# Kernel optimization log

Measured on AMD Instinct MI355X. Metric: run time of the kernel, lower is better.

## Reference

```python
import jax, jax.numpy as jnp
import numpy as np

HEADS = 8
DIM_HEADS = 64
M_DIM = 512
X_DIM = 512
MEM_NUM = 512
N = 16384
PERCENT = 0.25
LAY_NUMBER = 2       # outer refinement iterations
CROSS_LAYERS = 2     # layers inside M_cross_layers
EPS = 1e-5


def setup_inputs() -> dict:
    key = jax.random.key(0)
    ks = jax.random.split(key, 8)
    data = jax.random.normal(ks[0], (N, X_DIM), dtype=jnp.float32)
    Memory = jax.random.normal(ks[1], (MEM_NUM, M_DIM), dtype=jnp.float32)
    # to_kv: Linear(X_dim, 2*kv_dim, bias=False); kv_dim = heads*dim_heads
    Wkv = jax.random.normal(ks[2], (X_DIM, 2 * HEADS * DIM_HEADS), dtype=jnp.float32) * 0.02
    # per cross layer: to_q (no bias) and mutl_heads (with bias)
    Wq = jax.random.normal(ks[3], (CROSS_LAYERS, M_DIM, HEADS * DIM_HEADS), dtype=jnp.float32) * 0.02
    Wm = jax.random.normal(ks[4], (CROSS_LAYERS, HEADS * DIM_HEADS, M_DIM), dtype=jnp.float32) * 0.02
    bm = jnp.zeros((CROSS_LAYERS, M_DIM), dtype=jnp.float32)
    return {"data": data, "Memory": Memory, "Wkv": Wkv, "Wq": Wq, "Wm": Wm, "bm": bm, "istest": 0}


def _layer_norm(x):
    # F.layer_norm over last dim, no affine params
    mu = jnp.mean(x, axis=-1, keepdims=True)
    var = jnp.var(x, axis=-1, keepdims=True)
    return (x - mu) * jax.lax.rsqrt(var + EPS)


def _cross_layer(M, X, Wkv, Wq_l, Wm_l, bm_l):
    # cross_att + residual + layernorm (SublayerConnection); FFN is dead code in source
    q = (M @ Wq_l).reshape(MEM_NUM, HEADS, DIM_HEADS).transpose(1, 0, 2)      # [h, m, dh]
    kv = X @ Wkv                                                              # [n, 2*h*dh]
    k, v = jnp.split(kv, 2, axis=-1)
    k = k.reshape(-1, HEADS, DIM_HEADS).transpose(1, 0, 2)                    # [h, n, dh]
    v = v.reshape(-1, HEADS, DIM_HEADS).transpose(1, 0, 2)
    sim = jnp.einsum('hid,hjd->hij', q, k) * (DIM_HEADS ** -0.5)              # [h, m, n]
    att = jax.nn.softmax(sim, axis=-1)
    o = jnp.einsum('hij,hjd->hid', att, v)                                    # [h, m, dh]
    o = o.transpose(1, 0, 2).reshape(MEM_NUM, HEADS * DIM_HEADS)
    out = o @ Wm_l + bm_l                                                     # [m, M_dim]
    return _layer_norm(out + M)


def _cross_layers(M, X, Wkv, Wq, Wm, bm):
    for l in range(CROSS_LAYERS):
        M = _cross_layer(M, X, Wkv, Wq[l], Wm[l], bm[l])
    return M


def _calucate_sim(data, M):
    # per-sample landmark similarity: max scaled dot product against memory rows
    logits = (data @ M.T) * (DIM_HEADS ** -0.5)   # [N, mem]
    return jnp.max(logits, axis=-1)               # [N]


def _calucate_emb(data, M):
    logits = (data @ M.T) * (DIM_HEADS ** -0.5)   # [N, mem]
    logp = jax.nn.log_softmax(logits, axis=-1)
    p = jnp.exp(logp)
    out_ebs = p @ M                               # soft memory readout [N, M_dim]
    result_loss = -jnp.mean(jnp.max(logp, axis=-1))
    lse = jax.scipy.special.logsumexp(logits, axis=-1)
    zloss = jnp.mean(lse ** 2)                    # router-style z-loss
    return out_ebs, result_loss, zloss


def _select(data, sim_M, k):
    _, top_idx = jax.lax.top_k(sim_M, k)
    X = jnp.zeros_like(data)
    return X.at[top_idx].set(data[top_idx])


def reference(data, Memory, Wkv, Wq, Wm, bm, istest):
    M = Memory
    sim_M = _calucate_sim(data, M)
    percent_count = int(data.shape[0] * PERCENT)
    if not istest:
        X = _select(data, sim_M, percent_count)
        for _ in range(LAY_NUMBER):
            M = _cross_layers(M, X, Wkv, Wq, Wm, bm)
            sim_M = _calucate_sim(data, M)
            X = _select(data, sim_M, percent_count)
    out_ebs, result_loss, zloss = _calucate_emb(data, M)
    return (sim_M, out_ebs, result_loss, zloss)
```

## Files before the change

### kernel.cpp

```cpp
#include <hip/hip_runtime.h>
#include <cstdint>

#define N_DATA 16384
#define DIM 512
#define MEM 512
#define KSEL 4096
#define NH 8
#define DH 64
#define KVDIM 1024
#define SCALE 0.125f
#define ZCNT 12288.0f
#define LN_EPS 1e-5f
#define NSPLIT 4

typedef unsigned short u16;
using short8 = __attribute__((ext_vector_type(8))) short;
using f32x4  = __attribute__((ext_vector_type(4))) float;

__device__ __forceinline__ unsigned fenc(float x) {
    unsigned u = __float_as_uint(x);
    return (u & 0x80000000u) ? ~u : (u | 0x80000000u);
}
__device__ __forceinline__ u16 f2bf(float x) {
    unsigned u = __float_as_uint(x);
    u += 0x7fffu + ((u >> 16) & 1u);
    return (u16)(u >> 16);
}
__device__ __forceinline__ float bf2f(u16 h) { return __uint_as_float(((unsigned)h) << 16); }

__device__ __forceinline__ float waveSum(float v) {
#pragma unroll
    for (int o = 32; o > 0; o >>= 1) v += __shfl_down(v, o, 64);
    return v;
}
__device__ float blockSum(float v) {
    __shared__ float sh[4];
    __syncthreads();
    v = waveSum(v);
    if ((threadIdx.x & 63) == 0) sh[threadIdx.x >> 6] = v;
    __syncthreads();
    if (threadIdx.x == 0) { float s = sh[0]; for (int i = 1; i < 4; ++i) s += sh[i]; sh[0] = s; }
    __syncthreads();
    return sh[0];
}

template<int ROWS, int NW, bool GATHER>
__device__ __forceinline__ void stage_tile(const u16* __restrict__ src, int ld, int k0,
                                           int row0, const int* __restrict__ gidx,
                                           u16* lds, int wave)
{
    constexpr int NI = ROWS / 16;
    const int lane = threadIdx.x & 63;
#pragma unroll
    for (int i = wave; i < NI; i += NW) {
        const int ch = i * 64 + lane;
        const int r = ch >> 2, cc = ch & 3;
        int rg = row0 + r;
        if (GATHER) rg = gidx[rg];
        const u16* g = src + (long)rg * ld + k0 + cc * 8;
        u16* l = lds + i * 512;
        __builtin_amdgcn_global_load_lds((const __attribute__((address_space(1))) void*)g,
                                         (__attribute__((address_space(3))) void*)l,
                                         16, 0, 0);
    }
}

template<int WM, int WN, bool GATHER, int EPI, bool BIAS>
__global__ __launch_bounds__(WM * WN * 64)
void mfma_gemm(const u16* __restrict__ A, const u16* __restrict__ B,
               const float* __restrict__ bias, const int* __restrict__ gidx,
               void* __restrict__ Cv, unsigned* __restrict__ simenc,
               u16* __restrict__ vTo,
               int K, int lda, int ldb, int ldc,
               long zsA, long zsB, long zsC, int zdiv, long zsplitC, float alpha)
{
    constexpr int BM = WM * 64, BN = WN * 64, NW = WM * WN;
    __shared__ __align__(16) u16 As[BM * 32];
    __shared__ __align__(16) u16 Bs[BN * 32];

    const int t = threadIdx.x;
    const int wave = t >> 6, lane = t & 63;
    const int wr = wave / WN, wc = wave % WN;
    const int l15 = lane & 15, l4 = lane >> 4;
    const int bm0 = blockIdx.x * BM, bn0 = blockIdx.y * BN;
    const int zs = (int)blockIdx.z % zdiv;
    const int zh = (int)blockIdx.z / zdiv;
    A += (long)zh * zsA;
    B += (long)zh * zsB;

    f32x4 acc[4][4];
#pragma unroll
    for (int i = 0; i < 4; ++i)
#pragma unroll
        for (int j = 0; j < 4; ++j)
#pragma unroll
            for (int r = 0; r < 4; ++r) acc[i][j][r] = 0.f;

    const int Kd = K / zdiv;
    const int kbeg = zs * Kd;
    for (int k0 = kbeg; k0 < kbeg + Kd; k0 += 32) {
        stage_tile<BM, NW, GATHER>(A, lda, k0, bm0, gidx, As, wave);
        stage_tile<BN, NW, false>(B, ldb, k0, bn0, nullptr, Bs, wave);
        __syncthreads();
        short8 a[4], b[4];
#pragma unroll
        for (int fm = 0; fm < 4; ++fm)
            a[fm] = *(const short8*)(As + (wr * 64 + fm * 16 + l15) * 32 + l4 * 8);
#pragma unroll
        for (int fn = 0; fn < 4; ++fn)
            b[fn] = *(const short8*)(Bs + (wc * 64 + fn * 16 + l15) * 32 + l4 * 8);
#pragma unroll
        for (int fm = 0; fm < 4; ++fm)
#pragma unroll
            for (int fn = 0; fn < 4; ++fn)
                acc[fm][fn] = __builtin_amdgcn_mfma_f32_16x16x32_bf16(a[fm], b[fn], acc[fm][fn], 0, 0, 0);
        __syncthreads();
    }

    if (EPI == 2) {
#pragma unroll
        for (int fm = 0; fm < 4; ++fm)
#pragma unroll
            for (int r = 0; r < 4; ++r) {
                float mx = acc[fm][0][r];
#pragma unroll
                for (int fn = 1; fn < 4; ++fn) mx = fmaxf(mx, acc[fm][fn][r]);
#pragma unroll
                for (int o = 8; o >= 1; o >>= 1) mx = fmaxf(mx, __shfl_xor(mx, o, 64));
                if (l15 == 0) {
                    const int row = bm0 + wr * 64 + fm * 16 + l4 * 4 + r;
                    atomicMax(simenc + row, fenc(alpha * mx));
                }
            }
    } else if (EPI == 0) {
        float* C = (float*)Cv + (long)zh * zsC + (long)zs * zsplitC;
#pragma unroll
        for (int fm = 0; fm < 4; ++fm)
#pragma unroll
            for (int fn = 0; fn < 4; ++fn)
#pragma unroll
                for (int r = 0; r < 4; ++r) {
                    const int row = bm0 + wr * 64 + fm * 16 + l4 * 4 + r;
                    const int col = bn0 + wc * 64 + fn * 16 + l15;
                    float v = alpha * acc[fm][fn][r];
                    if (BIAS) v += bias[col];
                    C[(long)row * ldc + col] = v;
                }
    } else if (EPI == 1) {
        u16* C = (u16*)Cv + (long)zh * zsC + (long)zs * zsplitC;
#pragma unroll
        for (int fm = 0; fm < 4; ++fm)
#pragma unroll
            for (int fn = 0; fn < 4; ++fn)
#pragma unroll
                for (int r = 0; r < 4; ++r) {
                    const int row = bm0 + wr * 64 + fm * 16 + l4 * 4 + r;
                    const int col = bn0 + wc * 64 + fn * 16 + l15;
                    float v = alpha * acc[fm][fn][r];
                    if (BIAS) v += bias[col];
                    C[(long)row * ldc + col] = f2bf(v);
                }
    } else {
        if (bn0 < 512) {
            u16* C = (u16*)Cv;
#pragma unroll
            for (int fm = 0; fm < 4; ++fm)
#pragma unroll
                for (int fn = 0; fn < 4; ++fn)
#pragma unroll
                    for (int r = 0; r < 4; ++r) {
                        const int row = bm0 + wr * 64 + fm * 16 + l4 * 4 + r;
                        const int col = bn0 + wc * 64 + fn * 16 + l15;
                        C[(long)row * ldc + col] = f2bf(alpha * acc[fm][fn][r]);
                    }
        } else {
#pragma unroll
            for (int fm = 0; fm < 4; ++fm)
#pragma unroll
                for (int fn = 0; fn < 4; ++fn) {
                    const int d = bn0 + wc * 64 + fn * 16 + l15 - 512;
                    const int row0 = bm0 + wr * 64 + fm * 16 + l4 * 4;
                    ushort4 pw;
                    pw.x = f2bf(alpha * acc[fm][fn][0]);
                    pw.y = f2bf(alpha * acc[fm][fn][1]);
                    pw.z = f2bf(alpha * acc[fm][fn][2]);
                    pw.w = f2bf(alpha * acc[fm][fn][3]);
                    *(ushort4*)(vTo + (long)d * 4096 + row0) = pw;
                }
        }
    }
}

__global__ __launch_bounds__(512)
void mfma_gemm_sm(const u16* __restrict__ A, const u16* __restrict__ B,
                  u16* __restrict__ Obf, float* __restrict__ simf,
                  float* __restrict__ lse, float* __restrict__ mlp, float alpha)
{
    __shared__ __align__(16) u16 As[64 * 32];
    __shared__ __align__(16) u16 Bs[512 * 32];
    const int t = threadIdx.x, wave = t >> 6, lane = t & 63;
    const int wc = wave;
    const int l15 = lane & 15, l4 = lane >> 4;
    const int bm0 = blockIdx.x * 64;

    f32x4 acc[4][4];
#pragma unroll
    for (int i = 0; i < 4; ++i)
#pragma unroll
        for (int j = 0; j < 4; ++j)
#pragma unroll
            for (int r = 0; r < 4; ++r) acc[i][j][r] = 0.f;

    for (int k0 = 0; k0 < 512; k0 += 32) {
        stage_tile<64, 8, false>(A, 512, k0, bm0, nullptr, As, wave);
        stage_tile<512, 8, false>(B, 512, k0, 0, nullptr, Bs, wave);
        __syncthreads();
        short8 a[4], b[4];
#pragma unroll
        for (int fm = 0; fm < 4; ++fm)
            a[fm] = *(const short8*)(As + (fm * 16 + l15) * 32 + l4 * 8);
#pragma unroll
        for (int fn = 0; fn < 4; ++fn)
            b[fn] = *(const short8*)(Bs + (wc * 64 + fn * 16 + l15) * 32 + l4 * 8);
#pragma unroll
        for (int fm = 0; fm < 4; ++fm)
#pragma unroll
            for (int fn = 0; fn < 4; ++fn)
                acc[fm][fn] = __builtin_amdgcn_mfma_f32_16x16x32_bf16(a[fm], b[fn], acc[fm][fn], 0, 0, 0);
        __syncthreads();
    }

    float* red  = (float*)As;
    float* rowv = (float*)Bs;

#pragma unroll
    for (int fm = 0; fm < 4; ++fm)
#pragma unroll
        for (int r = 0; r < 4; ++r) {
            float mx = alpha * acc[fm][0][r];
#pragma unroll
            for (int fn = 1; fn < 4; ++fn) mx = fmaxf(mx, alpha * acc[fm][fn][r]);
#pragma unroll
            for (int o = 1; o <= 8; o <<= 1) mx = fmaxf(mx, __shfl_xor(mx, o, 64));
            if (l15 == 0) red[(fm * 16 + l4 * 4 + r) * 8 + wc] = mx;
        }
    __syncthreads();
    if (t < 64) {
        float mx = red[t * 8];
#pragma unroll
        for (int j = 1; j < 8; ++j) mx = fmaxf(mx, red[t * 8 + j]);
        rowv[t] = mx;
    }
    __syncthreads();
#pragma unroll
    for (int fm = 0; fm < 4; ++fm)
#pragma unroll
        for (int r = 0; r < 4; ++r) {
            const int rl = fm * 16 + l4 * 4 + r;
            const float m = rowv[rl];
            float s = 0.f;
#pragma unroll
            for (int fn = 0; fn < 4; ++fn) s += __expf(alpha * acc[fm][fn][r] - m);
#pragma unroll
            for (int o = 1; o <= 8; o <<= 1) s += __shfl_xor(s, o, 64);
            if (l15 == 0) red[rl * 8 + wc] = s;
        }
    __syncthreads();
    if (t < 64) {
        float s = 0.f;
#pragma unroll
        for (int j = 0; j < 8; ++j) s += red[t * 8 + j];
        const float m = rowv[t];
        const float l = m + __logf(s);
        const int gr = bm0 + t;
        simf[gr] = m; lse[gr] = l; mlp[gr] = m - l;
        rowv[64 + t] = l;
    }
    __syncthreads();
#pragma unroll
    for (int fm = 0; fm < 4; ++fm)
#pragma unroll
        for (int r = 0; r < 4; ++r) {
            const int rl = fm * 16 + l4 * 4 + r;
            const float l = rowv[64 + rl];
#pragma unroll
            for (int fn = 0; fn < 4; ++fn) {
                const int col = wc * 64 + fn * 16 + l15;
                Obf[(long)(bm0 + rl) * 512 + col] = f2bf(__expf(alpha * acc[fm][fn][r] - l));
            }
        }
}

__global__ __launch_bounds__(512)
void wmln(const u16* __restrict__ A, const u16* __restrict__ BT,
          const float* __restrict__ bias, const float* __restrict__ Min,
          float* __restrict__ Mout, u16* __restrict__ Mbf)
{
    __shared__ __align__(16) u16 As[16 * 32];
    __shared__ __align__(16) u16 Bs[512 * 32];
    __shared__ float red[16][8], red2[16][8], rowv[32];
    const int t = threadIdx.x, wave = t >> 6, lane = t & 63;
    const int wc = wave;
    const int l15 = lane & 15, l4 = lane >> 4;
    const int bm0 = blockIdx.x * 16;

    f32x4 acc[4];
#pragma unroll
    for (int fn = 0; fn < 4; ++fn)
#pragma unroll
        for (int r = 0; r < 4; ++r) acc[fn][r] = 0.f;

    for (int k0 = 0; k0 < 512; k0 += 32) {
        stage_tile<16, 8, false>(A, 512, k0, bm0, nullptr, As, wave);
        stage_tile<512, 8, false>(BT, 512, k0, 0, nullptr, Bs, wave);
        __syncthreads();
        const short8 a = *(const short8*)(As + l15 * 32 + l4 * 8);
#pragma unroll
        for (int fn = 0; fn < 4; ++fn) {
            const short8 b = *(const short8*)(Bs + (wc * 64 + fn * 16 + l15) * 32 + l4 * 8);
            acc[fn] = __builtin_amdgcn_mfma_f32_16x16x32_bf16(a, b, acc[fn], 0, 0, 0);
        }
        __syncthreads();
    }

    float v[4][4];
#pragma unroll
    for (int fn = 0; fn < 4; ++fn) {
        const int col = wc * 64 + fn * 16 + l15;
        const float bi = bias[col];
#pragma unroll
        for (int r = 0; r < 4; ++r) {
            const int row = bm0 + l4 * 4 + r;
            v[fn][r] = acc[fn][r] + bi + Min[(long)row * 512 + col];
        }
    }
#pragma unroll
    for (int r = 0; r < 4; ++r) {
        float s = 0.f, s2 = 0.f;
#pragma unroll
        for (int fn = 0; fn < 4; ++fn) { const float x = v[fn][r]; s += x; s2 += x * x; }
#pragma unroll
        for (int o = 1; o <= 8; o <<= 1) { s += __shfl_xor(s, o, 64); s2 += __shfl_xor(s2, o, 64); }
        if (l15 == 0) { red[l4 * 4 + r][wc] = s; red2[l4 * 4 + r][wc] = s2; }
    }
    __syncthreads();
    if (t < 16) {
        float s = 0.f, s2 = 0.f;
#pragma unroll
        for (int j = 0; j < 8; ++j) { s += red[t][j]; s2 += red2[t][j]; }
        const float mu = s * (1.f / 512.f);
        const float var = s2 * (1.f / 512.f) - mu * mu;
        rowv[t] = mu;
        rowv[16 + t] = rsqrtf(var + LN_EPS);
    }
    __syncthreads();
#pragma unroll
    for (int fn = 0; fn < 4; ++fn) {
        const int col = wc * 64 + fn * 16 + l15;
#pragma unroll
        for (int r = 0; r < 4; ++r) {
            const int rl = l4 * 4 + r;
            const float y = (v[fn][r] - rowv[rl]) * rowv[16 + rl];
            Mout[(long)(bm0 + rl) * 512 + col] = y;
            Mbf [(long)(bm0 + rl) * 512 + col] = f2bf(y);
        }
    }
}

__global__ __launch_bounds__(256)
void flash_att(const u16* __restrict__ Mbf, const u16* __restrict__ WqT,
               const u16* __restrict__ KV, const u16* __restrict__ VT,
               float* __restrict__ oPart, float* __restrict__ mPart,
               float* __restrict__ lPart)
{
    __shared__ __align__(16) u16 Qs[64 * 64];
    __shared__ __align__(16) u16 Ks[2][64 * 64];
    __shared__ __align__(16) u16 Vs[2][64 * 64];
    __shared__ __align__(16) u16 Ps[4][16 * 72];

    const int qt = blockIdx.x, h = blockIdx.y, sp = blockIdx.z;
    const int t = threadIdx.x, wave = t >> 6, lane = t & 63;
    const int l15 = lane & 15, l4 = lane >> 4;

    const u16* Kg = KV + ((long)sp * 1024) * 1024 + h * 64;
    const u16* Vg = VT + ((long)h * 64) * 4096 + sp * 1024;

    auto stageKV = [&](int kt, int buf) {
        const u16* Kt = Kg + (long)(kt * 64) * 1024;
        const u16* Vt = Vg + kt * 64;
#pragma unroll
        for (int i = wave; i < 8; i += 4) {
            const int ch = i * 64 + lane, r = ch >> 3, s = ch & 7;
            __builtin_amdgcn_global_load_lds(
                (const __attribute__((address_space(1))) void*)(Kt + (long)r * 1024 + ((s ^ (r & 7)) * 8)),
                (__attribute__((address_space(3))) void*)(Ks[buf] + i * 512), 16, 0, 0);
        }
#pragma unroll
        for (int i = wave; i < 8; i += 4) {
            const int ch = i * 64 + lane, r = ch >> 3, s = ch & 7;
            __builtin_amdgcn_global_load_lds(
                (const __attribute__((address_space(1))) void*)(Vt + (long)r * 4096 + ((s ^ (r & 7)) * 8)),
                (__attribute__((address_space(3))) void*)(Vs[buf] + i * 512), 16, 0, 0);
        }
    };

    stageKV(0, 0);

    f32x4 accq[4];
#pragma unroll
    for (int fn = 0; fn < 4; ++fn)
#pragma unroll
        for (int r = 0; r < 4; ++r) accq[fn][r] = 0.f;
    {
        const u16* Ag = Mbf + (long)(qt * 64 + wave * 16 + l15) * 512 + l4 * 8;
        const u16* Bg = WqT + (long)(h * 64 + l15) * 512 + l4 * 8;
#pragma unroll 4
        for (int k0 = 0; k0 < 512; k0 += 32) {
            const short8 a = *(const short8*)(Ag + k0);
#pragma unroll
            for (int fn = 0; fn < 4; ++fn) {
                const short8 b = *(const short8*)(Bg + (long)fn * 16 * 512 + k0);
                accq[fn] = __builtin_amdgcn_mfma_f32_16x16x32_bf16(a, b, accq[fn], 0, 0, 0);
            }
        }
    }
#pragma unroll
    for (int fn = 0; fn < 4; ++fn)
#pragma unroll
        for (int r = 0; r < 4; ++r) {
            const int qrow = wave * 16 + l4 * 4 + r;
            const int col = fn * 16 + l15;
            Qs[qrow * 64 + (((col >> 3) ^ (qrow & 7)) << 3) + (col & 7)] = f2bf(accq[fn][r]);
        }
    __syncthreads();

    const int qr = wave * 16 + l15;
    short8 qf0 = *(const short8*)(Qs + qr * 64 + ((0 * 4 + l4) ^ (qr & 7)) * 8);
    short8 qf1 = *(const short8*)(Qs + qr * 64 + ((1 * 4 + l4) ^ (qr & 7)) * 8);

    float m = -3.0e38f, lsum = 0.f;
    f32x4 acc_o[4];
#pragma unroll
    for (int nf = 0; nf < 4; ++nf)
#pragma unroll
        for (int r = 0; r < 4; ++r) acc_o[nf][r] = 0.f;

    u16* myP = &Ps[wave][0];
    constexpr int NT = KSEL / 64 / NSPLIT;
    int cur = 0;

    for (int kt = 0; kt < NT; ++kt) {
        if (kt + 1 < NT) stageKV(kt + 1, cur ^ 1);
        const u16* Kc = Ks[cur];
        const u16* Vc = Vs[cur];
        f32x4 acc_s[4];
#pragma unroll
        for (int mf = 0; mf < 4; ++mf) {
#pragma unroll
            for (int r = 0; r < 4; ++r) acc_s[mf][r] = 0.f;
            const int kr = mf * 16 + l15;
            const short8 ka0 = *(const short8*)(Kc + kr * 64 + ((0 * 4 + l4) ^ (kr & 7)) * 8);
            const short8 ka1 = *(const short8*)(Kc + kr * 64 + ((1 * 4 + l4) ^ (kr & 7)) * 8);
            acc_s[mf] = __builtin_amdgcn_mfma_f32_16x16x32_bf16(ka0, qf0, acc_s[mf], 0, 0, 0);
            acc_s[mf] = __builtin_amdgcn_mfma_f32_16x16x32_bf16(ka1, qf1, acc_s[mf], 0, 0, 0);
        }
        float sv[16];
#pragma unroll
        for (int mf = 0; mf < 4; ++mf)
#pragma unroll
            for (int r = 0; r < 4; ++r) sv[mf * 4 + r] = SCALE * acc_s[mf][r];
        float pm = sv[0];
#pragma unroll
        for (int j = 1; j < 16; ++j) pm = fmaxf(pm, sv[j]);
        pm = fmaxf(pm, __shfl_xor(pm, 16, 64));
        pm = fmaxf(pm, __shfl_xor(pm, 32, 64));
        const float mnew = fmaxf(m, pm);
        const float corr = __expf(m - mnew);
        float rs = 0.f;
#pragma unroll
        for (int j = 0; j < 16; ++j) { sv[j] = __expf(sv[j] - mnew); rs += sv[j]; }
        rs += __shfl_xor(rs, 16, 64);
        rs += __shfl_xor(rs, 32, 64);
        lsum = lsum * corr + rs;
        m = mnew;
        const float cf0 = __shfl(corr, l4 * 4 + 0, 64);
        const float cf1 = __shfl(corr, l4 * 4 + 1, 64);
        const float cf2 = __shfl(corr, l4 * 4 + 2, 64);
        const float cf3 = __shfl(corr, l4 * 4 + 3, 64);
#pragma unroll
        for (int nf = 0; nf < 4; ++nf) {
            acc_o[nf][0] *= cf0; acc_o[nf][1] *= cf1;
            acc_o[nf][2] *= cf2; acc_o[nf][3] *= cf3;
        }
#pragma unroll
        for (int mf = 0; mf < 4; ++mf) {
            ushort4 pw;
            pw.x = f2bf(sv[mf * 4 + 0]); pw.y = f2bf(sv[mf * 4 + 1]);
            pw.z = f2bf(sv[mf * 4 + 2]); pw.w = f2bf(sv[mf * 4 + 3]);
            *(ushort4*)(myP + l15 * 72 + mf * 16 + l4 * 4) = pw;
        }
#pragma unroll
        for (int ks = 0; ks < 2; ++ks) {
            const short8 pa = *(const short8*)(myP + l15 * 72 + ks * 32 + l4 * 8);
#pragma unroll
            for (int nf = 0; nf < 4; ++nf) {
                const int dr = nf * 16 + l15;
                const short8 vb = *(const short8*)(Vc + dr * 64 + ((ks * 4 + l4) ^ (dr & 7)) * 8);
                acc_o[nf] = __builtin_amdgcn_mfma_f32_16x16x32_bf16(pa, vb, acc_o[nf], 0, 0, 0);
            }
        }
        __syncthreads();
        cur ^= 1;
    }

    float* ob = oPart + (((long)sp * NH + h) * 8 + qt) * 4096;
#pragma unroll
    for (int nf = 0; nf < 4; ++nf)
#pragma unroll
        for (int r = 0; r < 4; ++r)
            ob[(wave * 16 + l4 * 4 + r) * 64 + nf * 16 + l15] = acc_o[nf][r];
    if (lane < 16) {
        const int qi = wave * 16 + lane;
        mPart[((sp * NH + h) * 8 + qt) * 64 + qi] = m;
        lPart[((sp * NH + h) * 8 + qt) * 64 + qi] = lsum;
    }
}

__global__ __launch_bounds__(256)
void flash_combine(const float* __restrict__ oPart, const float* __restrict__ mPart,
                   const float* __restrict__ lPart, u16* __restrict__ o_bf)
{
    const int qt = blockIdx.x & 7, h = blockIdx.x >> 3;
    const int t = threadIdx.x;
    const int q = t >> 2, d0 = (t & 3) << 4;
    float mi[NSPLIT], li[NSPLIT];
#pragma unroll
    for (int sp = 0; sp < NSPLIT; ++sp) {
        const int sb = ((sp * NH + h) * 8 + qt) * 64 + q;
        mi[sp] = mPart[sb];
        li[sp] = lPart[sb];
    }
    float ms = 0.f;
#pragma unroll
    for (int sp = 0; sp < NSPLIT; ++sp) ms = fmaxf(ms, mi[sp]);
    float denom = ZCNT * __expf(-ms);
    float f[NSPLIT];
#pragma unroll
    for (int sp = 0; sp < NSPLIT; ++sp) { f[sp] = __expf(mi[sp] - ms); denom += li[sp] * f[sp]; }
    const float inv = 1.f / denom;
    float o[16];
#pragma unroll
    for (int j = 0; j < 16; ++j) o[j] = 0.f;
#pragma unroll
    for (int sp = 0; sp < NSPLIT; ++sp) {
        const float* ob = oPart + (((long)sp * NH + h) * 8 + qt) * 4096 + q * 64 + d0;
        const float fs = f[sp] * inv;
#pragma unroll
        for (int j = 0; j < 16; j += 4) {
            const float4 v = *(const float4*)(ob + j);
            o[j] += fs * v.x; o[j + 1] += fs * v.y; o[j + 2] += fs * v.z; o[j + 3] += fs * v.w;
        }
    }
    u16* op = o_bf + (qt * 64 + q) * 512 + h * 64 + d0;
#pragma unroll
    for (int j = 0; j < 16; j += 4) {
        ushort4 w4;
        w4.x = f2bf(o[j]); w4.y = f2bf(o[j + 1]); w4.z = f2bf(o[j + 2]); w4.w = f2bf(o[j + 3]);
        *(ushort4*)(op + j) = w4;
    }
}

#define PRO_DATA 8192
#define PRO_W4   1024
#define PRO_WKV  512
#define PRO_MEM  256
__global__ __launch_bounds__(256)
void prologue(const float* __restrict__ data, const float* __restrict__ Memory,
              const float* __restrict__ Wkv, const float* __restrict__ Wq,
              const float* __restrict__ Wm,
              u16* __restrict__ data_bf, u16* __restrict__ Mbf,
              u16* __restrict__ WkvT, u16* __restrict__ WqT, u16* __restrict__ WmT)
{
    __shared__ float tile[32][33];
    const int bid = blockIdx.x, t = threadIdx.x;
    if (bid < PRO_DATA) {
        const int i = (bid * 256 + t) * 4;
        const float4 v = *(const float4*)(data + i);
        ushort4 o;
        o.x = f2bf(v.x); o.y = f2bf(v.y); o.z = f2bf(v.z); o.w = f2bf(v.w);
        *(ushort4*)(data_bf + i) = o;
        return;
    }
    int b2 = bid - PRO_DATA;
    const int tx = t & 31, ty = t >> 5;
    if (b2 < PRO_W4) {
        const int z = b2 >> 8, q = b2 & 255;
        const float* S = (z < 2) ? (Wq + (long)z * DIM * DIM) : (Wm + (long)(z - 2) * DIM * DIM);
        u16* D = (z < 2) ? (WqT + (long)z * DIM * DIM) : (WmT + (long)(z - 2) * DIM * DIM);
        const int c0 = (q & 15) * 32, r0 = (q >> 4) * 32;
#pragma unroll
        for (int j = 0; j < 32; j += 8)
            tile[ty + j][tx] = S[(long)(r0 + ty + j) * DIM + c0 + tx];
        __syncthreads();
#pragma unroll
        for (int j = 0; j < 32; j += 8)
            D[(long)(c0 + ty + j) * DIM + r0 + tx] = f2bf(tile[tx][ty + j]);
        return;
    }
    b2 -= PRO_W4;
    if (b2 < PRO_WKV) {
        const int c0 = (b2 & 31) * 32, r0 = (b2 >> 5) * 32;
#pragma unroll
        for (int j = 0; j < 32; j += 8)
            tile[ty + j][tx] = Wkv[(long)(r0 + ty + j) * KVDIM + c0 + tx];
        __syncthreads();
#pragma unroll
        for (int j = 0; j < 32; j += 8)
            WkvT[(long)(c0 + ty + j) * DIM + r0 + tx] = f2bf(tile[tx][ty + j]);
        return;
    }
    b2 -= PRO_WKV;
    {
        const int i = (b2 * 256 + t) * 4;
        const float4 v = *(const float4*)(Memory + i);
        ushort4 o;
        o.x = f2bf(v.x); o.y = f2bf(v.y); o.z = f2bf(v.z); o.w = f2bf(v.w);
        *(ushort4*)(Mbf + i) = o;
    }
}

__global__ __launch_bounds__(256)
void transpose_f32bf(const float* __restrict__ S, u16* __restrict__ D, int Rr, int ldS)
{
    __shared__ float tile[32][33];
    const int c0 = blockIdx.x * 32, r0 = blockIdx.y * 32;
    const int tx = threadIdx.x & 31, ty = threadIdx.x >> 5;
#pragma unroll
    for (int j = 0; j < 32; j += 8)
        tile[ty + j][tx] = S[(long)(r0 + ty + j) * ldS + c0 + tx];
    __syncthreads();
#pragma unroll
    for (int j = 0; j < 32; j += 8)
        D[(long)(c0 + ty + j) * Rr + r0 + tx] = f2bf(tile[tx][ty + j]);
}

__device__ __forceinline__ unsigned scan1024_excl(unsigned v, unsigned* wsum)
{
    const int lane = threadIdx.x & 63, wv = threadIdx.x >> 6;
    __syncthreads();
    unsigned x = v;
#pragma unroll
    for (int o = 1; o < 64; o <<= 1) {
        unsigned y = __shfl_up(x, o, 64);
        if (lane >= o) x += y;
    }
    if (lane == 63) wsum[wv] = x;
    __syncthreads();
    if (threadIdx.x < 16) {
        unsigned w2 = wsum[threadIdx.x];
#pragma unroll
        for (int o = 1; o < 16; o <<= 1) {
            unsigned y = __shfl_up(w2, o, 64);
            if ((int)threadIdx.x >= o) w2 += y;
        }
        wsum[threadIdx.x] = w2;
    }
    __syncthreads();
    const unsigned off = (wv > 0) ? wsum[wv - 1] : 0u;
    return off + x - v;
}

#define SEL_T 1024
#define SEL_CH (N_DATA / SEL_T)
__global__ __launch_bounds__(SEL_T)
void select_topk(const unsigned* __restrict__ key, int* __restrict__ idxo, int k)
{
    __shared__ unsigned whist[16][256];
    __shared__ unsigned hist[256];
    __shared__ unsigned wsum[16];
    __shared__ unsigned sh_bin, sh_r;
    const int t = threadIdx.x;
    const int wv = t >> 6;
    const int base = t * SEL_CH;

    unsigned kreg[SEL_CH];
#pragma unroll
    for (int c = 0; c < SEL_CH; ++c) kreg[c] = key[base + c];

    unsigned prefix = 0, mask = 0;
    unsigned r = (unsigned)k;
    for (int p = 3; p >= 0; --p) {
        __syncthreads();
        for (int i = t; i < 16 * 256; i += SEL_T) ((unsigned*)whist)[i] = 0u;
        __syncthreads();
#pragma unroll
        for (int c = 0; c < SEL_CH; ++c) {
            const unsigned kv = kreg[c];
            if ((kv & mask) == prefix)
                atomicAdd(&whist[wv][(kv >> (p * 8)) & 255u], 1u);
        }
        __syncthreads();
        if (t < 256) {
            unsigned s = 0;
#pragma unroll
            for (int wq = 0; wq < 16; ++wq) s += whist[wq][t];
            hist[t] = s;
        }
        __syncthreads();
        if (t < 64) {
            const int b0 = 255 - 4 * t;
            const unsigned c = hist[b0] + hist[b0 - 1] + hist[b0 - 2] + hist[b0 - 3];
            unsigned x = c;
#pragma unroll
            for (int o = 1; o < 64; o <<= 1) {
                unsigned y = __shfl_up(x, o, 64);
                if (t >= o) x += y;
            }
            const unsigned pre = x - c;
            if (pre < r && r <= x) {
                unsigned cum = pre;
#pragma unroll
                for (int j = 0; j < 4; ++j) {
                    const int b = b0 - j;
                    cum += hist[b];
                    if (cum >= r) { sh_bin = (unsigned)b; sh_r = r - (cum - hist[b]); break; }
                }
            }
        }
        __syncthreads();
        prefix |= sh_bin << (p * 8);
        mask |= 255u << (p * 8);
        r = sh_r;
    }
    const unsigned thr = prefix;
    const unsigned ties = r;

    unsigned ceq = 0;
#pragma unroll
    for (int c = 0; c < SEL_CH; ++c) ceq += (kreg[c] == thr) ? 1u : 0u;
    const unsigned eqbase = scan1024_excl(ceq, wsum);
    unsigned eq = eqbase, csel = 0;
#pragma unroll
    for (int c = 0; c < SEL_CH; ++c) {
        const unsigned kv = kreg[c];
        bool s;
        if (kv == thr) { s = (eq < ties); ++eq; }
        else s = (kv > thr);
        csel += s ? 1u : 0u;
    }
    unsigned pos = scan1024_excl(csel, wsum);
    eq = eqbase;
#pragma unroll
    for (int c = 0; c < SEL_CH; ++c) {
        const unsigned kv = kreg[c];
        bool s;
        if (kv == thr) { s = (eq < ties); ++eq; }
        else s = (kv > thr);
        if (s) idxo[pos++] = base + c;
    }
}

__global__ __launch_bounds__(256)
void reduce_loss(const float* __restrict__ lse, const float* __restrict__ mlp,
                 float* __restrict__ o2)
{
    const int t = threadIdx.x;
    float s1 = 0.f, s2 = 0.f;
    for (int i = t; i < N_DATA; i += 256) { s1 += mlp[i]; float l = lse[i]; s2 += l * l; }
    s1 = blockSum(s1);
    s2 = blockSum(s2);
    if (t == 0) { o2[0] = -s1 * (1.f / N_DATA); o2[1] = s2 * (1.f / N_DATA); }
}

extern "C" void kernel_launch(void* const* d_in, const int* in_sizes, int n_in,
                              void* d_out, int out_size, void* d_ws, size_t ws_size,
                              hipStream_t stream)
{
    (void)in_sizes; (void)n_in; (void)out_size; (void)ws_size;
    const float* data   = (const float*)d_in[0];
    const float* Memory = (const float*)d_in[1];
    const float* Wkv    = (const float*)d_in[2];
    const float* Wq     = (const float*)d_in[3];
    const float* Wm     = (const float*)d_in[4];
    const float* bm     = (const float*)d_in[5];
    float* out = (float*)d_out;

    char* w = (char*)d_ws;
    unsigned* simenc = (unsigned*)(w + 0);
    int*   idx     = (int*)  (w + 65536);
    float* lse     = (float*)(w + 81920);
    float* mlp     = (float*)(w + 147456);
    float* Ma      = (float*)(w + 262144);
    float* Mb      = (float*)(w + 1310720);
    u16*   Mbf0    = (u16*)  (w + 2359296);
    u16*   MT_bf   = (u16*)  (w + 2883584);
    u16*   WqT_bf  = (u16*)  (w + 3407872);
    u16*   WmT_bf  = (u16*)  (w + 4456448);
    u16*   WkvT_bf = (u16*)  (w + 5505024);
    u16*   o_bf    = (u16*)  (w + 7077888);
    u16*   data_bf = (u16*)  (w + 8650752);
    u16*   kvsel_bf= (u16*)  (w + 25427968);
    u16*   vT_bf   = (u16*)  (w + 33816576);
    float* oPart   = (float*)(w + 38010880);
    float* mPart   = (float*)(w + 42205184);
    float* lPart   = (float*)(w + 42270720);
    u16*   logits_bf = (u16*)(w + 54788096);
    u16*   Mbfa    = (u16*)  (w + 88342528);
    u16*   Mbfb    = (u16*)  (w + 88866816);

    prologue<<<PRO_DATA + PRO_W4 + PRO_WKV + PRO_MEM, 256, 0, stream>>>(
        data, Memory, Wkv, Wq, Wm, data_bf, Mbf0, WkvT_bf, WqT_bf, WmT_bf);

    auto sim_select_kv = [&](const u16* Mrows_bf) {
        hipMemsetAsync(simenc, 0, N_DATA * 4, stream);
        mfma_gemm<2, 2, false, 2, false><<<dim3(128, 4, 1), 256, 0, stream>>>(
            data_bf, Mrows_bf, nullptr, nullptr, nullptr, simenc, nullptr,
            DIM, DIM, DIM, 0, 0, 0, 0, 1, 0, SCALE);
        select_topk<<<1, SEL_T, 0, stream>>>(simenc, idx, KSEL);
        mfma_gemm<2, 2, true, 3, false><<<dim3(32, 8, 1), 256, 0, stream>>>(
            data_bf, WkvT_bf, nullptr, idx, kvsel_bf, nullptr, vT_bf,
            DIM, DIM, DIM, KVDIM, 0, 0, 0, 1, 0, 1.0f);
    };

    auto cross = [&](const float* Mcur, const u16* Mcur_bf, float* Mnext, u16* Mnext_bf, int l) {
        flash_att<<<dim3(8, NH, NSPLIT), 256, 0, stream>>>(
            Mcur_bf, WqT_bf + (long)l * DIM * DIM, kvsel_bf, vT_bf, oPart, mPart, lPart);
        flash_combine<<<64, 256, 0, stream>>>(oPart, mPart, lPart, o_bf);
        wmln<<<32, 512, 0, stream>>>(
            o_bf, WmT_bf + (long)l * DIM * DIM, bm + (long)l * DIM, Mcur, Mnext, Mnext_bf);
    };

    const float* Mcur = Memory;
    const u16*  curbf = Mbf0;
    float* Mnext = Ma;
    u16*   nextbf = Mbfa;
    sim_select_kv(curbf);
    for (int it = 0; it < 2; ++it) {
        for (int l = 0; l < 2; ++l) {
            cross(Mcur, curbf, Mnext, nextbf, l);
            Mcur = Mnext; curbf = nextbf;
            Mnext = (Mcur == Ma) ? Mb : Ma;
            nextbf = (curbf == Mbfa) ? Mbfb : Mbfa;
        }
        if (it == 0) sim_select_kv(curbf);
    }

    mfma_gemm_sm<<<N_DATA / 64, 512, 0, stream>>>(
        data_bf, curbf, logits_bf, out, lse, mlp, SCALE);
    transpose_f32bf<<<dim3(16, 16), 256, 0, stream>>>(Mcur, MT_bf, MEM, DIM);
    mfma_gemm<2, 2, false, 0, false><<<dim3(128, 4, 1), 256, 0, stream>>>(
        logits_bf, MT_bf, nullptr, nullptr, out + N_DATA, nullptr, nullptr,
        MEM, MEM, MEM, DIM, 0, 0, 0, 1, 0, 1.0f);
    reduce_loss<<<1, 256, 0, stream>>>(lse, mlp, out + N_DATA + (long)N_DATA * DIM);
}
```

Baseline: 381.6 us.

## Double K-step in GEMM, split flash attention 8 ways, fuse memsets and transpose

The generic MFMA GEMM now stages two 32-wide K slices per barrier pair, halving the number of synchronisations at the cost of doubled LDS. Flash attention splits the selected keys 8 ways instead of 4 for more parallel blocks, so the partial buffers are relocated. The simenc zeroing moves from hipMemsetAsync into the prologue and the wmln kernel, and the final memory transpose to bf16 is fused into the last wmln epilogue, removing two launches. The transposed store in wmln is strided and uncoalesced, and the extra LDS may lower occupancy.

After: 398.1 us. 4.3% more time.

```diff
diff --git a/kernel.cpp b/kernel.cpp
--- a/kernel.cpp
+++ b/kernel.cpp
@@ -11,7 +11,8 @@
 #define SCALE 0.125f
 #define ZCNT 12288.0f
 #define LN_EPS 1e-5f
-#define NSPLIT 4
+#define NSPLIT 8
+#define ROWS_SP (KSEL / NSPLIT)
 
 typedef unsigned short u16;
 using short8 = __attribute__((ext_vector_type(8))) short;
@@ -76,7 +77,9 @@
 {
     constexpr int BM = WM * 64, BN = WN * 64, NW = WM * WN;
     __shared__ __align__(16) u16 As[BM * 32];
+    __shared__ __align__(16) u16 As2[BM * 32];
     __shared__ __align__(16) u16 Bs[BN * 32];
+    __shared__ __align__(16) u16 Bs2[BN * 32];
 
     const int t = threadIdx.x;
     const int wave = t >> 6, lane = t & 63;
@@ -98,22 +101,40 @@
 
     const int Kd = K / zdiv;
     const int kbeg = zs * Kd;
-    for (int k0 = kbeg; k0 < kbeg + Kd; k0 += 32) {
+    for (int k0 = kbeg; k0 < kbeg + Kd; k0 += 64) {
         stage_tile<BM, NW, GATHER>(A, lda, k0, bm0, gidx, As, wave);
+        stage_tile<BM, NW, GATHER>(A, lda, k0 + 32, bm0, gidx, As2, wave);
         stage_tile<BN, NW, false>(B, ldb, k0, bn0, nullptr, Bs, wave);
-        __syncthreads();
-        short8 a[4], b[4];
-#pragma unroll
-        for (int fm = 0; fm < 4; ++fm)
-            a[fm] = *(const short8*)(As + (wr * 64 + fm * 16 + l15) * 32 + l4 * 8);
-#pragma unroll
-        for (int fn = 0; fn < 4; ++fn)
-            b[fn] = *(const short8*)(Bs + (wc * 64 + fn * 16 + l15) * 32 + l4 * 8);
-#pragma unroll
-        for (int fm = 0; fm < 4; ++fm)
+        stage_tile<BN, NW, false>(B, ldb, k0 + 32, bn0, nullptr, Bs2, wave);
+        __syncthreads();
+        {
+            short8 a[4], b[4];
+#pragma unroll
+            for (int fm = 0; fm < 4; ++fm)
+                a[fm] = *(const short8*)(As + (wr * 64 + fm * 16 + l15) * 32 + l4 * 8);
 #pragma unroll
             for (int fn = 0; fn < 4; ++fn)
-                acc[fm][fn] = __builtin_amdgcn_mfma_f32_16x16x32_bf16(a[fm], b[fn], acc[fm][fn], 0, 0, 0);
+                b[fn] = *(const short8*)(Bs + (wc * 64 + fn * 16 + l15) * 32 + l4 * 8);
+#pragma unroll
+            for (int fm = 0; fm < 4; ++fm)
+#pragma unroll
+                for (int fn = 0; fn < 4; ++fn)
+                    acc[fm][fn] = __builtin_amdgcn_mfma_f32_16x16x32_bf16(a[fm], b[fn], acc[fm][fn], 0, 0, 0);
+        }
+        {
+            short8 a[4], b[4];
+#pragma unroll
+            for (int fm = 0; fm < 4; ++fm)
+                a[fm] = *(const short8*)(As2 + (wr * 64 + fm * 16 + l15) * 32 + l4 * 8);
+#pragma unroll
+            for (int fn = 0; fn < 4; ++fn)
+                b[fn] = *(const short8*)(Bs2 + (wc * 64 + fn * 16 + l15) * 32 + l4 * 8);
+#pragma unroll
+            for (int fm = 0; fm < 4; ++fm)
+#pragma unroll
+                for (int fn = 0; fn < 4; ++fn)
+                    acc[fm][fn] = __builtin_amdgcn_mfma_f32_16x16x32_bf16(a[fm], b[fn], acc[fm][fn], 0, 0, 0);
+        }
         __syncthreads();
     }
 
@@ -294,7 +315,8 @@
 __global__ __launch_bounds__(512)
 void wmln(const u16* __restrict__ A, const u16* __restrict__ BT,
           const float* __restrict__ bias, const float* __restrict__ Min,
-          float* __restrict__ Mout, u16* __restrict__ Mbf)
+          float* __restrict__ Mout, u16* __restrict__ Mbf,
+          unsigned* __restrict__ simz, u16* __restrict__ MTout)
 {
     __shared__ __align__(16) u16 As[16 * 32];
     __shared__ __align__(16) u16 Bs[512 * 32];
@@ -304,6 +326,8 @@
     const int l15 = lane & 15, l4 = lane >> 4;
     const int bm0 = blockIdx.x * 16;
 
+    simz[blockIdx.x * 512 + t] = 0u;
+
     f32x4 acc[4];
 #pragma unroll
     for (int fn = 0; fn < 4; ++fn)
@@ -363,6 +387,7 @@
             const float y = (v[fn][r] - rowv[rl]) * rowv[16 + rl];
             Mout[(long)(bm0 + rl) * 512 + col] = y;
             Mbf [(long)(bm0 + rl) * 512 + col] = f2bf(y);
+            if (MTout) MTout[(long)col * 512 + (bm0 + rl)] = f2bf(y);
         }
     }
 }
@@ -382,8 +407,8 @@
     const int t = threadIdx.x, wave = t >> 6, lane = t & 63;
     const int l15 = lane & 15, l4 = lane >> 4;
 
-    const u16* Kg = KV + ((long)sp * 1024) * 1024 + h * 64;
-    const u16* Vg = VT + ((long)h * 64) * 4096 + sp * 1024;
+    const u16* Kg = KV + ((long)sp * ROWS_SP) * 1024 + h * 64;
+    const u16* Vg = VT + ((long)h * 64) * 4096 + sp * ROWS_SP;
 
     auto stageKV = [&](int kt, int buf) {
         const u16* Kt = Kg + (long)(kt * 64) * 1024;
@@ -446,7 +471,7 @@
         for (int r = 0; r < 4; ++r) acc_o[nf][r] = 0.f;
 
     u16* myP = &Ps[wave][0];
-    constexpr int NT = KSEL / 64 / NSPLIT;
+    constexpr int NT = ROWS_SP / 64;
     int cur = 0;
 
     for (int kt = 0; kt < NT; ++kt) {
@@ -574,12 +599,14 @@
 #define PRO_W4   1024
 #define PRO_WKV  512
 #define PRO_MEM  256
+#define PRO_SIM  16
 __global__ __launch_bounds__(256)
 void prologue(const float* __restrict__ data, const float* __restrict__ Memory,
               const float* __restrict__ Wkv, const float* __restrict__ Wq,
               const float* __restrict__ Wm,
               u16* __restrict__ data_bf, u16* __restrict__ Mbf,
-              u16* __restrict__ WkvT, u16* __restrict__ WqT, u16* __restrict__ WmT)
+              u16* __restrict__ WkvT, u16* __restrict__ WqT, u16* __restrict__ WmT,
+              unsigned* __restrict__ simenc)
 {
     __shared__ float tile[32][33];
     const int bid = blockIdx.x, t = threadIdx.x;
@@ -620,28 +647,20 @@
         return;
     }
     b2 -= PRO_WKV;
-    {
+    if (b2 < PRO_MEM) {
         const int i = (b2 * 256 + t) * 4;
         const float4 v = *(const float4*)(Memory + i);
         ushort4 o;
         o.x = f2bf(v.x); o.y = f2bf(v.y); o.z = f2bf(v.z); o.w = f2bf(v.w);
         *(ushort4*)(Mbf + i) = o;
-    }
-}
-
-__global__ __launch_bounds__(256)
-void transpose_f32bf(const float* __restrict__ S, u16* __restrict__ D, int Rr, int ldS)
-{
-    __shared__ float tile[32][33];
-    const int c0 = blockIdx.x * 32, r0 = blockIdx.y * 32;
-    const int tx = threadIdx.x & 31, ty = threadIdx.x >> 5;
-#pragma unroll
-    for (int j = 0; j < 32; j += 8)
-        tile[ty + j][tx] = S[(long)(r0 + ty + j) * ldS + c0 + tx];
-    __syncthreads();
-#pragma unroll
-    for (int j = 0; j < 32; j += 8)
-        D[(long)(c0 + ty + j) * Rr + r0 + tx] = f2bf(tile[tx][ty + j]);
+        return;
+    }
+    b2 -= PRO_MEM;
+    {
+        const int i = (b2 * 256 + t) * 4;
+        uint4 z; z.x = z.y = z.z = z.w = 0u;
+        *(uint4*)(simenc + i) = z;
+    }
 }
 
 __device__ __forceinline__ unsigned scan1024_excl(unsigned v, unsigned* wsum)
@@ -802,17 +821,16 @@
     u16*   kvsel_bf= (u16*)  (w + 25427968);
     u16*   vT_bf   = (u16*)  (w + 33816576);
     float* oPart   = (float*)(w + 38010880);
-    float* mPart   = (float*)(w + 42205184);
-    float* lPart   = (float*)(w + 42270720);
+    float* mPart   = (float*)(w + 46399488);
+    float* lPart   = (float*)(w + 46530560);
     u16*   logits_bf = (u16*)(w + 54788096);
     u16*   Mbfa    = (u16*)  (w + 88342528);
     u16*   Mbfb    = (u16*)  (w + 88866816);
 
-    prologue<<<PRO_DATA + PRO_W4 + PRO_WKV + PRO_MEM, 256, 0, stream>>>(
-        data, Memory, Wkv, Wq, Wm, data_bf, Mbf0, WkvT_bf, WqT_bf, WmT_bf);
+    prologue<<<PRO_DATA + PRO_W4 + PRO_WKV + PRO_MEM + PRO_SIM, 256, 0, stream>>>(
+        data, Memory, Wkv, Wq, Wm, data_bf, Mbf0, WkvT_bf, WqT_bf, WmT_bf, simenc);
 
     auto sim_select_kv = [&](const u16* Mrows_bf) {
-        hipMemsetAsync(simenc, 0, N_DATA * 4, stream);
         mfma_gemm<2, 2, false, 2, false><<<dim3(128, 4, 1), 256, 0, stream>>>(
             data_bf, Mrows_bf, nullptr, nullptr, nullptr, simenc, nullptr,
             DIM, DIM, DIM, 0, 0, 0, 0, 1, 0, SCALE);
@@ -822,12 +840,14 @@
             DIM, DIM, DIM, KVDIM, 0, 0, 0, 1, 0, 1.0f);
     };
 
-    auto cross = [&](const float* Mcur, const u16* Mcur_bf, float* Mnext, u16* Mnext_bf, int l) {
+    auto cross = [&](const float* Mcur, const u16* Mcur_bf, float* Mnext, u16* Mnext_bf,
+                     int l, u16* MTout) {
         flash_att<<<dim3(8, NH, NSPLIT), 256, 0, stream>>>(
             Mcur_bf, WqT_bf + (long)l * DIM * DIM, kvsel_bf, vT_bf, oPart, mPart, lPart);
         flash_combine<<<64, 256, 0, stream>>>(oPart, mPart, lPart, o_bf);
         wmln<<<32, 512, 0, stream>>>(
-            o_bf, WmT_bf + (long)l * DIM * DIM, bm + (long)l * DIM, Mcur, Mnext, Mnext_bf);
+            o_bf, WmT_bf + (long)l * DIM * DIM, bm + (long)l * DIM, Mcur,
+            Mnext, Mnext_bf, simenc, MTout);
     };
 
     const float* Mcur = Memory;
@@ -837,7 +857,8 @@
     sim_select_kv(curbf);
     for (int it = 0; it < 2; ++it) {
         for (int l = 0; l < 2; ++l) {
-            cross(Mcur, curbf, Mnext, nextbf, l);
+            const bool last = (it == 1 && l == 1);
+            cross(Mcur, curbf, Mnext, nextbf, l, last ? MT_bf : nullptr);
             Mcur = Mnext; curbf = nextbf;
             Mnext = (Mcur == Ma) ? Mb : Ma;
             nextbf = (curbf == Mbfa) ? Mbfb : Mbfa;
@@ -847,7 +868,6 @@
 
     mfma_gemm_sm<<<N_DATA / 64, 512, 0, stream>>>(
         data_bf, curbf, logits_bf, out, lse, mlp, SCALE);
-    transpose_f32bf<<<dim3(16, 16), 256, 0, stream>>>(Mcur, MT_bf, MEM, DIM);
     mfma_gemm<2, 2, false, 0, false><<<dim3(128, 4, 1), 256, 0, stream>>>(
         logits_bf, MT_bf, nullptr, nullptr, out + N_DATA, nullptr, nullptr,
         MEM, MEM, MEM, DIM, 0, 0, 0, 1, 0, 1.0f);
```
